# Optimization experiments

Measured on AMD Instinct MI355X. Metric: run time of the kernel, lower is better.

Reference implementation:

```python
import jax, jax.numpy as jnp
import numpy as np

K = 2  # num_selected_experts
NOISE_STD = 1.0

def setup_inputs() -> dict:
    key = jax.random.key(0)
    k1, k2, k3, k4 = jax.random.split(key, 4)
    G, S, H, E = 32, 1024, 2048, 64
    tokens = jax.random.normal(k1, (G, S, H), dtype=jnp.float32)
    noise = jax.random.normal(k2, (G * S, E), dtype=jnp.float32) * NOISE_STD
    # nn.Linear(H, E): weight (E, H), bias (E); kaiming-uniform-ish scale
    lim = 1.0 / np.sqrt(H)
    W = jax.random.uniform(k3, (E, H), dtype=jnp.float32, minval=-lim, maxval=lim)
    b = jax.random.uniform(k4, (E,), dtype=jnp.float32, minval=-lim, maxval=lim)
    return {"tokens": tokens, "noise": noise, "W": W, "b": b}

def reference(tokens, noise, W, b):
    G, S, H = tokens.shape
    E = W.shape[0]
    flat = tokens.reshape(G * S, H)
    # linear projection + pre-sampled gaussian noise (training mode)
    logits = jnp.einsum('nh,eh->ne', flat, W) + b + noise  # (G*S, E)
    probs = jax.nn.softmax(logits, axis=-1)
    kk = min(K, E)
    topk_vals, topk_idx = jax.lax.top_k(probs, kk)  # (G*S, k)
    topk_w = topk_vals / (topk_vals.sum(axis=-1, keepdims=True) + 1e-9)
    # aux loss stats over experts
    importance = probs.sum(axis=0)                     # (E,)
    load = (probs > 0).astype(jnp.float32).sum(axis=0) # (E,)
    aux_loss = jnp.var(importance * load, ddof=1) * 0.01  # torch .var() is unbiased
    return (topk_idx.reshape(G, S, kk),
            topk_w.reshape(G, S, kk),
            aux_loss,
            probs.reshape(G, S, E))
```

## Files before the change

### kernel.cpp

```cpp
#include <hip/hip_runtime.h>


constexpr int GS    = 32768;
constexpr int EXPN  = 64;
constexpr int HID   = 2048;
constexpr int BM    = 64;
constexpr int KHALF = 1024;
constexpr int NCH   = KHALF / 32;
constexpr int BUFB  = 16384;

typedef __attribute__((ext_vector_type(8))) short s16x8;
typedef __attribute__((ext_vector_type(4))) float f32x4;

#define AS_GLOBAL(p) ((const __attribute__((address_space(1))) void*)(p))
#define AS_LDS(p)    ((__attribute__((address_space(3))) void*)(p))

__device__ __forceinline__ void decomp8(float4 x0, float4 x1, s16x8& h, s16x8& m)
{
    float v[8] = {x0.x,x0.y,x0.z,x0.w,x1.x,x1.y,x1.z,x1.w};
    #pragma unroll
    for (int i = 0; i < 8; ++i) {
        union { float f; unsigned u; } a; a.f = v[i];
        unsigned hb = (a.u + 0x7fffu + ((a.u >> 16) & 1u)) >> 16;
        union { unsigned u; float f; } hf; hf.u = hb << 16;
        float r = (v[i] - hf.f) * 256.f;
        union { float f; unsigned u; } rb; rb.f = r;
        h[i] = (short)hb;
        m[i] = (short)(rb.u >> 16);
    }
}

__global__ __launch_bounds__(256)
void prep_kernel(const float* __restrict__ W, short* __restrict__ WhF,
                 short* __restrict__ WmF)
{
    const int t  = blockIdx.x * 256 + threadIdx.x;
    const int cs = t >> 8;
    const int nt = (t >> 6) & 3;
    const int l  = t & 63;
    const int e  = nt * 16 + (l & 15);
    const int kb = cs * 32 + ((l >> 4) << 3);
    const float* p = W + (size_t)e * HID + kb;
    float4 x0 = *(const float4*)p;
    float4 x1 = *(const float4*)(p + 4);
    s16x8 h, m;
    decomp8(x0, x1, h, m);
    *(s16x8*)&WhF[(size_t)t * 8] = h;
    *(s16x8*)&WmF[(size_t)t * 8] = m;
}

__global__ __launch_bounds__(512, 2)
void router_kernel(const float* __restrict__ tokens,
                   const float* __restrict__ noise,
                   const float* __restrict__ bias,
                   const short* __restrict__ WhF,
                   const short* __restrict__ WmF,
                   float* __restrict__ out,
                   float* __restrict__ ws)
{
    __shared__ __align__(16) char smem[2 * BUFB];

    const int tid  = threadIdx.x;
    const int lane = tid & 63;
    const int wv   = tid >> 6;
    const int mt   = wv & 3;
    const int kh   = wv >> 2;
    const int row0 = blockIdx.x * BM;

    const float* Ap = tokens
        + (size_t)(row0 + mt * 16 + (lane & 15)) * HID
        + kh * KHALF + ((lane >> 4) << 3);

    auto stage = [&](int b, int c) {
        char* base = smem + b * BUFB;
        #pragma unroll
        for (int i = 0; i < 2; ++i) {
            const int r    = wv * 2 + i;
            const int half = r >> 3;
            const int hm   = (r >> 2) & 1;
            const int nt   = r & 3;
            const int cs   = half * NCH + c;
            const short* src = (hm ? WmF : WhF)
                + ((size_t)cs * 256 + nt * 64 + lane) * 8;
            __builtin_amdgcn_global_load_lds(AS_GLOBAL(src),
                                             AS_LDS(base + r * 1024), 16, 0, 0);
        }
    };

    f32x4 accM[4], accS[4];
    #pragma unroll
    for (int nt = 0; nt < 4; ++nt) { accM[nt] = (f32x4)0.f; accS[nt] = (f32x4)0.f; }

    float4 aA0 = *(const float4*)(Ap);
    float4 aA1 = *(const float4*)(Ap + 4);
    float4 aB0, aB1;
    stage(0, 0);
    __syncthreads();

#define CHUNK(A0, A1, N0, N1, c)                                                   \
    {                                                                              \
        const int bc = (c) & 1;                                                    \
        if ((c) + 1 < NCH) {                                                       \
            stage(bc ^ 1, (c) + 1);                                                \
            N0 = *(const float4*)(Ap + ((c) + 1) * 32);                            \
            N1 = *(const float4*)(Ap + ((c) + 1) * 32 + 4);                        \
        }                                                                          \
        const char* wb = smem + bc * BUFB + kh * 8192;                             \
        s16x8 ah, am;                                                              \
        decomp8(A0, A1, ah, am);                                                   \
        _Pragma("unroll")                                                          \
        for (int nt = 0; nt < 4; ++nt) {                                           \
            s16x8 bh = *(const s16x8*)(wb + nt * 1024 + lane * 16);                \
            s16x8 bm = *(const s16x8*)(wb + 4096 + nt * 1024 + lane * 16);         \
            accM[nt] = __builtin_amdgcn_mfma_f32_16x16x32_bf16(ah, bh, accM[nt], 0, 0, 0); \
            accS[nt] = __builtin_amdgcn_mfma_f32_16x16x32_bf16(ah, bm, accS[nt], 0, 0, 0); \
            accS[nt] = __builtin_amdgcn_mfma_f32_16x16x32_bf16(am, bh, accS[nt], 0, 0, 0); \
        }                                                                          \
        __syncthreads();              \
    }

    for (int c = 0; c < NCH; c += 2) {
        CHUNK(aA0, aA1, aB0, aB1, c);
        CHUNK(aB0, aB1, aA0, aA1, c + 1);
    }
#undef CHUNK

    float (*lg)[EXPN + 1] = (float (*)[EXPN + 1])smem;
    float (*red)[EXPN]    = (float (*)[EXPN])(smem + BM * (EXPN + 1) * 4);

    if (kh == 0) {
        #pragma unroll
        for (int nt = 0; nt < 4; ++nt)
            #pragma unroll
            for (int r = 0; r < 4; ++r)
                lg[mt * 16 + (lane >> 4) * 4 + r][nt * 16 + (lane & 15)]
                    = accM[nt][r] + 0.00390625f * accS[nt][r];
    }
    __syncthreads();
    if (kh == 1) {
        #pragma unroll
        for (int nt = 0; nt < 4; ++nt)
            #pragma unroll
            for (int r = 0; r < 4; ++r)
                lg[mt * 16 + (lane >> 4) * 4 + r][nt * 16 + (lane & 15)]
                    += accM[nt][r] + 0.00390625f * accS[nt][r];
    }
    __syncthreads();

    float* out_idx   = out;
    float* out_w     = out + 2 * GS;
    float* out_probs = out + 4 * GS + 1;

    const float blane = bias[lane];
    float impL = 0.f, cntL = 0.f;

    for (int rr = 0; rr < 8; ++rr) {
        const int r = (wv << 3) + rr;
        const size_t row = (size_t)row0 + r;
        float v = lg[r][lane] + blane + noise[row * EXPN + lane];

        float m = v;
        #pragma unroll
        for (int off = 32; off >= 1; off >>= 1)
            m = fmaxf(m, __shfl_xor(m, off));
        float e = expf(v - m);
        float s = e;
        #pragma unroll
        for (int off = 32; off >= 1; off >>= 1)
            s += __shfl_xor(s, off);
        float p = e / s;

        out_probs[row * EXPN + lane] = p;
        impL += p;
        cntL += (p > 0.f) ? 1.f : 0.f;

        float v1 = p; int i1 = lane;
        #pragma unroll
        for (int off = 32; off >= 1; off >>= 1) {
            float ov = __shfl_xor(v1, off);
            int   oi = __shfl_xor(i1, off);
            if (ov > v1 || (ov == v1 && oi < i1)) { v1 = ov; i1 = oi; }
        }
        float v2 = (lane == i1) ? -1.f : p; int i2 = lane;
        #pragma unroll
        for (int off = 32; off >= 1; off >>= 1) {
            float ov = __shfl_xor(v2, off);
            int   oi = __shfl_xor(i2, off);
            if (ov > v2 || (ov == v2 && oi < i2)) { v2 = ov; i2 = oi; }
        }
        if (lane == 0) {
            float denom = v1 + v2 + 1e-9f;
            out_idx[row * 2 + 0] = (float)i1;
            out_idx[row * 2 + 1] = (float)i2;
            out_w[row * 2 + 0] = v1 / denom;
            out_w[row * 2 + 1] = v2 / denom;
        }
    }

    red[wv][lane]     = impL;
    red[8 + wv][lane] = cntL;
    __syncthreads();
    if (tid < EXPN) {
        float t1 = 0.f, t2 = 0.f;
        #pragma unroll
        for (int w = 0; w < 8; ++w) { t1 += red[w][tid]; t2 += red[8 + w][tid]; }
        atomicAdd(&ws[tid], t1);
        atomicAdd(&ws[EXPN + tid], t2);
    }
}

__global__ void aux_kernel(const float* __restrict__ ws, float* __restrict__ out)
{
    const int lane = threadIdx.x;
    float x = ws[lane] * ws[EXPN + lane];
    float s = x;
    #pragma unroll
    for (int off = 32; off >= 1; off >>= 1)
        s += __shfl_xor(s, off);
    float mean = s * (1.f / 64.f);
    float d = x - mean;
    float ss = d * d;
    #pragma unroll
    for (int off = 32; off >= 1; off >>= 1)
        ss += __shfl_xor(ss, off);
    if (lane == 0)
        out[4 * GS] = 0.01f * (ss / 63.f);
}

extern "C" void kernel_launch(void* const* d_in, const int* in_sizes, int n_in,
                              void* d_out, int out_size, void* d_ws, size_t ws_size,
                              hipStream_t stream)
{
    const float* tokens = (const float*)d_in[0];
    const float* noise  = (const float*)d_in[1];
    const float* W      = (const float*)d_in[2];
    const float* bias   = (const float*)d_in[3];
    float* out = (float*)d_out;
    float* ws  = (float*)d_ws;

    short* WhF = (short*)(ws + 128);
    short* WmF = WhF + (size_t)EXPN * HID;

    hipMemsetAsync(ws, 0, 2 * EXPN * sizeof(float), stream);
    prep_kernel<<<EXPN * HID / 8 / 256, 256, 0, stream>>>(W, WhF, WmF);
    router_kernel<<<GS / BM, 512, 0, stream>>>(tokens, noise, bias, WhF, WmF,
                                               out, ws);
    aux_kernel<<<1, 64, 0, stream>>>(ws, out);
}
```

Measured before the change: 85.82 us.

## Double K-chunk size per pipeline stage and fold workspace zeroing into prep kernel

Each pipeline stage now covers 64 K-elements instead of 32, so the LDS double buffer grows to 32KB per buffer and barriers per K-half are halved. Two float4 pairs of activations are prefetched per stage, which deepens the in-flight memory traffic. The memset that zeroes the workspace accumulators is moved into the prep kernel, removing one launch. The larger LDS footprint (64KB per block) and extra registers may limit occupancy at two blocks per CU.

Result: no change. 86.22 us (+0.5%).

```diff
diff --git a/kernel.cpp b/kernel.cpp
--- a/kernel.cpp
+++ b/kernel.cpp
@@ -6,8 +6,9 @@
 constexpr int HID   = 2048;
 constexpr int BM    = 64;
 constexpr int KHALF = 1024;
-constexpr int NCH   = KHALF / 32;
-constexpr int BUFB  = 16384;
+constexpr int NSUB  = KHALF / 32;
+constexpr int NCH   = KHALF / 64;
+constexpr int BUFB  = 32768;
 
 typedef __attribute__((ext_vector_type(8))) short s16x8;
 typedef __attribute__((ext_vector_type(4))) float f32x4;
@@ -32,8 +33,11 @@
 
 __global__ __launch_bounds__(256)
 void prep_kernel(const float* __restrict__ W, short* __restrict__ WhF,
-                 short* __restrict__ WmF)
-{
+                 short* __restrict__ WmF, float* __restrict__ ws)
+{
+    if (blockIdx.x == 0 && threadIdx.x < 2 * EXPN)
+        ws[threadIdx.x] = 0.f;
+
     const int t  = blockIdx.x * 256 + threadIdx.x;
     const int cs = t >> 8;
     const int nt = (t >> 6) & 3;
@@ -74,12 +78,13 @@
     auto stage = [&](int b, int c) {
         char* base = smem + b * BUFB;
         #pragma unroll
-        for (int i = 0; i < 2; ++i) {
-            const int r    = wv * 2 + i;
-            const int half = r >> 3;
+        for (int i = 0; i < 4; ++i) {
+            const int r    = wv * 4 + i;
+            const int half = r >> 4;
+            const int sub  = (r >> 3) & 1;
             const int hm   = (r >> 2) & 1;
             const int nt   = r & 3;
-            const int cs   = half * NCH + c;
+            const int cs   = half * NSUB + c * 2 + sub;
             const short* src = (hm ? WmF : WhF)
                 + ((size_t)cs * 256 + nt * 64 + lane) * 8;
             __builtin_amdgcn_global_load_lds(AS_GLOBAL(src),
@@ -93,19 +98,23 @@
 
     float4 aA0 = *(const float4*)(Ap);
     float4 aA1 = *(const float4*)(Ap + 4);
-    float4 aB0, aB1;
+    float4 aA2 = *(const float4*)(Ap + 32);
+    float4 aA3 = *(const float4*)(Ap + 36);
+    float4 aB0, aB1, aB2, aB3;
     stage(0, 0);
     __syncthreads();
 
-#define CHUNK(A0, A1, N0, N1, c)                                                   \
+#define CHUNK(A0, A1, A2, A3, N0, N1, N2, N3, c)                                   \
     {                                                                              \
         const int bc = (c) & 1;                                                    \
         if ((c) + 1 < NCH) {                                                       \
             stage(bc ^ 1, (c) + 1);                                                \
-            N0 = *(const float4*)(Ap + ((c) + 1) * 32);                            \
-            N1 = *(const float4*)(Ap + ((c) + 1) * 32 + 4);                        \
+            N0 = *(const float4*)(Ap + ((c) + 1) * 64);                            \
+            N1 = *(const float4*)(Ap + ((c) + 1) * 64 + 4);                        \
+            N2 = *(const float4*)(Ap + ((c) + 1) * 64 + 32);                       \
+            N3 = *(const float4*)(Ap + ((c) + 1) * 64 + 36);                       \
         }                                                                          \
-        const char* wb = smem + bc * BUFB + kh * 8192;                             \
+        const char* wb = smem + bc * BUFB + kh * 16384;                            \
         s16x8 ah, am;                                                              \
         decomp8(A0, A1, ah, am);                                                   \
         _Pragma("unroll")                                                          \
@@ -116,12 +125,21 @@
             accS[nt] = __builtin_amdgcn_mfma_f32_16x16x32_bf16(ah, bm, accS[nt], 0, 0, 0); \
             accS[nt] = __builtin_amdgcn_mfma_f32_16x16x32_bf16(am, bh, accS[nt], 0, 0, 0); \
         }                                                                          \
+        decomp8(A2, A3, ah, am);                                                   \
+        _Pragma("unroll")                                                          \
+        for (int nt = 0; nt < 4; ++nt) {                                           \
+            s16x8 bh = *(const s16x8*)(wb + 8192 + nt * 1024 + lane * 16);         \
+            s16x8 bm = *(const s16x8*)(wb + 8192 + 4096 + nt * 1024 + lane * 16);  \
+            accM[nt] = __builtin_amdgcn_mfma_f32_16x16x32_bf16(ah, bh, accM[nt], 0, 0, 0); \
+            accS[nt] = __builtin_amdgcn_mfma_f32_16x16x32_bf16(ah, bm, accS[nt], 0, 0, 0); \
+            accS[nt] = __builtin_amdgcn_mfma_f32_16x16x32_bf16(am, bh, accS[nt], 0, 0, 0); \
+        }                                                                          \
         __syncthreads();              \
     }
 
     for (int c = 0; c < NCH; c += 2) {
-        CHUNK(aA0, aA1, aB0, aB1, c);
-        CHUNK(aB0, aB1, aA0, aA1, c + 1);
+        CHUNK(aA0, aA1, aA2, aA3, aB0, aB1, aB2, aB3, c);
+        CHUNK(aB0, aB1, aB2, aB3, aA0, aA1, aA2, aA3, c + 1);
     }
 #undef CHUNK
 
@@ -241,8 +259,7 @@
     short* WhF = (short*)(ws + 128);
     short* WmF = WhF + (size_t)EXPN * HID;
 
-    hipMemsetAsync(ws, 0, 2 * EXPN * sizeof(float), stream);
-    prep_kernel<<<EXPN * HID / 8 / 256, 256, 0, stream>>>(W, WhF, WmF);
+    prep_kernel<<<EXPN * HID / 8 / 256, 256, 0, stream>>>(W, WhF, WmF, ws);
     router_kernel<<<GS / BM, 512, 0, stream>>>(tokens, noise, bias, WhF, WmF,
                                                out, ws);
     aux_kernel<<<1, 64, 0, stream>>>(ws, out);
```
